# Kernel tuning notes

Hardware: AMD Instinct MI355X
Metric: run time of the kernel (lower is better)

## Reference

```python
import jax, jax.numpy as jnp
import numpy as np

ALPHA = 0.5      # GCN2Conv alpha
THETA = 1.0      # GCN2Conv theta (beta_l = log(theta/l + 1))
EPS = 1e-5       # pyg LayerNorm eps
N_LAYERS = 8
N, E, DIN, DHID, DOUT = 50000, 800000, 128, 256, 128


def setup_inputs() -> dict:
    key = jax.random.key(0)
    ks = jax.random.split(key, 10)
    x = jax.random.normal(ks[0], (N, DIN), jnp.float32)
    edge_index = jax.random.randint(ks[1], (2, E), 0, N, dtype=jnp.int32)
    lin1_w = jax.random.normal(ks[2], (DIN, DHID), jnp.float32) / np.sqrt(DIN)
    lin1_b = jnp.zeros((DHID,), jnp.float32)
    conv_w1 = jax.random.normal(ks[3], (N_LAYERS, DHID, DHID), jnp.float32) / np.sqrt(DHID)
    conv_w2 = jax.random.normal(ks[4], (N_LAYERS, DHID, DHID), jnp.float32) / np.sqrt(DHID)
    norm_gamma = jnp.ones((N_LAYERS, DHID), jnp.float32)
    norm_beta = jnp.zeros((N_LAYERS, DHID), jnp.float32)
    lin2_w = jax.random.normal(ks[5], (DHID, DOUT), jnp.float32) / np.sqrt(DHID)
    lin2_b = jnp.zeros((DOUT,), jnp.float32)
    return {"x": x, "edge_index": edge_index, "lin1_w": lin1_w, "lin1_b": lin1_b,
            "conv_w1": conv_w1, "conv_w2": conv_w2, "norm_gamma": norm_gamma,
            "norm_beta": norm_beta, "lin2_w": lin2_w, "lin2_b": lin2_b}


def _gcn_norm(edge_index, n_nodes, dtype):
    # add self loops, then symmetric deg^{-1/2} A_hat deg^{-1/2} normalization
    loop = jnp.arange(n_nodes, dtype=edge_index.dtype)
    row = jnp.concatenate([edge_index[0], loop])
    col = jnp.concatenate([edge_index[1], loop])
    deg = jax.ops.segment_sum(jnp.ones_like(row, dtype=dtype), col, num_segments=n_nodes)
    dis = jnp.where(deg > 0, jax.lax.rsqrt(jnp.maximum(deg, 1e-12)), 0.0)
    return row, col, dis[row] * dis[col]


def _graph_layernorm(h, gamma, beta):
    # pyg LayerNorm mode='graph', batch=None: normalize over all nodes+features
    z = h - jnp.mean(h)
    z = z / (jnp.sqrt(jnp.mean(z * z)) + EPS)
    return gamma * z + beta


def reference(x, edge_index, lin1_w, lin1_b, conv_w1, conv_w2, norm_gamma, norm_beta, lin2_w, lin2_b):
    n_nodes = x.shape[0]
    row, col, enorm = _gcn_norm(edge_index, n_nodes, x.dtype)
    # lin1 + relu (dropout p=0 -> identity); residual=None -> zeros
    x0 = jax.nn.relu(x @ lin1_w + lin1_b)
    h = x0
    for i in range(conv_w1.shape[0]):
        beta_l = float(np.log(THETA / (i + 1) + 1.0))
        # sparse neighborhood aggregation: out[c] += norm * h[r]
        agg = jax.ops.segment_sum(h[row] * enorm[:, None], col, num_segments=n_nodes)
        t = (1.0 - ALPHA) * agg          # propagated part
        r = ALPHA * x0                   # initial-residual part (res = x0 + zeros)
        # shared_weights=False: separate weights for propagated and residual parts
        h = (1.0 - beta_l) * (t + r) + beta_l * (t @ conv_w1[i] + r @ conv_w2[i])
        h = jax.nn.relu(_graph_layernorm(h, norm_gamma[i], norm_beta[i]))
    return jax.nn.relu(h @ lin2_w + lin2_b)
```

## Files before the change

kernel.cpp:

```cpp
#include <hip/hip_runtime.h>
#include <hip/hip_bf16.h>
#include <math.h>

#define DIN 128
#define DH 256
#define DOUT 128
#define NLAYERS 8
#define EPSLN 1e-5f

typedef __hip_bfloat16 bf16;
typedef __attribute__((ext_vector_type(8))) short short8;
typedef __attribute__((ext_vector_type(4))) short short4v;
typedef __attribute__((ext_vector_type(4))) float f32x4;

__device__ __forceinline__ float ldf(const void* p, size_t idx, int isbf) {
    if (isbf) return __bfloat162float(((const bf16*)p)[idx]);
    return ((const float*)p)[idx];
}
__device__ __forceinline__ short f2s(float v) {
    bf16 b = __float2bfloat16(v);
    return *reinterpret_cast<short*>(&b);
}
__device__ __forceinline__ float s2f(short s) {
    unsigned int u = ((unsigned int)(unsigned short)s) << 16;
    float f;
    __builtin_memcpy(&f, &u, 4);
    return f;
}
__device__ __forceinline__ void gl_lds16(const void* g, void* l) {
    __builtin_amdgcn_global_load_lds(
        (const __attribute__((address_space(1))) unsigned int*)g,
        (__attribute__((address_space(3))) unsigned int*)l,
        16, 0, 0);
}

__global__ void k_detect(const unsigned int* __restrict__ xw, int* __restrict__ flag) {
    __shared__ int cnt;
    if (threadIdx.x == 0) cnt = 0;
    __syncthreads();
    unsigned int w = xw[threadIdx.x];
    int e = (w >> 7) & 0xFF;
    if (e >= 112 && e <= 140) atomicAdd(&cnt, 1);
    __syncthreads();
    if (threadIdx.x == 0) *flag = (cnt >= 128) ? 1 : 0;
}

__global__ void k_init_cnt(int* __restrict__ cnt, int N) {
    int i = blockIdx.x * blockDim.x + threadIdx.x;
    if (i < N) cnt[i] = 0;
}
__global__ void k_count(const int* __restrict__ cols, int* __restrict__ cnt, int E) {
    int e = blockIdx.x * blockDim.x + threadIdx.x;
    if (e < E) atomicAdd(&cnt[cols[e]], 1);
}
__global__ void k_dis(const int* __restrict__ cnt, float* __restrict__ dis, int N) {
    int i = blockIdx.x * blockDim.x + threadIdx.x;
    if (i < N) dis[i] = rsqrtf(1.0f + (float)cnt[i]);
}
__global__ void k_scan1(const int* __restrict__ cnt, int* __restrict__ rowptr,
                        int* __restrict__ bsum, int N) {
    __shared__ int s[256];
    int t = threadIdx.x;
    int i = blockIdx.x * 256 + t;
    s[t] = (i < N) ? cnt[i] : 0;
    __syncthreads();
    for (int off = 1; off < 256; off <<= 1) {
        int x = (t >= off) ? s[t - off] : 0;
        __syncthreads();
        s[t] += x;
        __syncthreads();
    }
    if (i < N) rowptr[i + 1] = s[t];
    if (t == 255) bsum[blockIdx.x] = s[255];
}
__global__ void k_scan2(int* __restrict__ bsum, int nb) {
    __shared__ int s[256];
    int t = threadIdx.x;
    s[t] = (t < nb) ? bsum[t] : 0;
    __syncthreads();
    for (int off = 1; off < 256; off <<= 1) {
        int x = (t >= off) ? s[t - off] : 0;
        __syncthreads();
        s[t] += x;
        __syncthreads();
    }
    if (t < nb) bsum[t] = s[t];
}
__global__ void k_scan3(int* __restrict__ rowptr, const int* __restrict__ bsum, int N) {
    int i = blockIdx.x * 256 + threadIdx.x;
    if (i == 0) rowptr[0] = 0;
    if (i < N && blockIdx.x > 0) rowptr[i + 1] += bsum[blockIdx.x - 1];
}
__global__ void k_cursor(const int* __restrict__ rowptr, int* __restrict__ cursor, int N) {
    int i = blockIdx.x * 256 + threadIdx.x;
    if (i < N) cursor[i] = rowptr[i];
}
__global__ void k_fill(const int* __restrict__ rows, const int* __restrict__ cols,
                       int* __restrict__ cursor, int* __restrict__ csr, int E) {
    int e = blockIdx.x * blockDim.x + threadIdx.x;
    if (e < E) {
        int c = cols[e], r = rows[e];
        int pos = atomicAdd(&cursor[c], 1);
        csr[pos] = r;
    }
}

__global__ void k_zero_stats(float* __restrict__ stats) {
    int t = threadIdx.x;
    if (t < 16) stats[t] = 0.0f;
}

__global__ void k_transw2(const void* __restrict__ w1, const void* __restrict__ w2,
                          const int* __restrict__ flag, short* __restrict__ wt) {
    __shared__ float tile[32][33];
    int z = blockIdx.z;
    int lay = z >> 1, m = z & 1;
    const void* src = m ? w2 : w1;
    size_t sbase = (size_t)lay * 65536;
    short* dst = wt + (size_t)lay * 131072 + (size_t)m * 256;
    float bl = logf(1.0f / (float)(lay + 1) + 1.0f);
    float c0 = 0.5f * (1.0f - bl);
    float c1 = 0.5f * bl;
    int isbf = *flag;
    int tx = threadIdx.x, ty = threadIdx.y;
    int n0 = blockIdx.x * 32, k0 = blockIdx.y * 32;
    #pragma unroll
    for (int i = 0; i < 4; i++) {
        int k = k0 + ty + i * 8;
        tile[ty + i * 8][tx] = ldf(src, sbase + (size_t)k * 256 + n0 + tx, isbf);
    }
    __syncthreads();
    #pragma unroll
    for (int i = 0; i < 4; i++) {
        int n = n0 + ty + i * 8;
        int k = k0 + tx;
        float v = c1 * tile[tx][ty + i * 8];
        if (k == n) v += c0;
        dst[(size_t)n * 512 + k] = f2s(v);
    }
}

__global__ void k_transw_lin(const void* __restrict__ src, const int* __restrict__ flag,
                             short* __restrict__ dst, int K, int Nc) {
    __shared__ float tile[32][33];
    int isbf = *flag;
    int tx = threadIdx.x, ty = threadIdx.y;
    int n0 = blockIdx.x * 32, k0 = blockIdx.y * 32;
    #pragma unroll
    for (int i = 0; i < 4; i++) {
        int k = k0 + ty + i * 8;
        tile[ty + i * 8][tx] = ldf(src, (size_t)k * Nc + n0 + tx, isbf);
    }
    __syncthreads();
    #pragma unroll
    for (int i = 0; i < 4; i++) {
        int n = n0 + ty + i * 8;
        dst[(size_t)n * K + k0 + tx] = f2s(tile[tx][ty + i * 8]);
    }
}

__global__ void k_convx(const void* __restrict__ x, const int* __restrict__ flag,
                        short* __restrict__ xb, int total) {
    int i = blockIdx.x * 256 + threadIdx.x;
    if (i < total) xb[i] = f2s(ldf(x, i, *flag));
}

template<int BN, int KK, int FINAL>
__global__ __launch_bounds__(256) void gemm_mfma(
    const short* __restrict__ A, const short* __restrict__ wt,
    const void* __restrict__ bias, const int* __restrict__ flag,
    void* __restrict__ outp, int Nn)
{
    constexpr int NT = BN / 16;
    __shared__ __align__(16) short Atile[128 * 32];
    __shared__ __align__(16) short Btile[BN * 32];
    int t = threadIdx.x;
    int w = t >> 6, lane = t & 63;
    int lr = lane & 15, quad = lane >> 4;
    int row0 = blockIdx.x * 128;
    int sub = t & 3;
    int srow = t >> 2;
    f32x4 acc[2][NT];
    #pragma unroll
    for (int m = 0; m < 2; m++)
        #pragma unroll
        for (int nt = 0; nt < NT; nt++)
            #pragma unroll
            for (int j = 0; j < 4; j++) acc[m][nt][j] = 0.f;

    for (int kb = 0; kb < KK; kb += 32) {
        #pragma unroll
        for (int r = 0; r < 2; r++) {
            int gr = row0 + srow + r * 64;
            if (gr >= Nn) gr = Nn - 1;
            gl_lds16(A + (size_t)gr * KK + kb + sub * 8,
                     Atile + (size_t)(t + r * 256) * 8);
        }
        #pragma unroll
        for (int r = 0; r < BN / 64; r++) {
            int n = srow + r * 64;
            gl_lds16(wt + (size_t)n * KK + kb + sub * 8,
                     Btile + (size_t)(t + r * 256) * 8);
        }
        __syncthreads();
        short8 a0 = *(const short8*)(Atile + (w * 32 + lr) * 32 + quad * 8);
        short8 a1 = *(const short8*)(Atile + (w * 32 + 16 + lr) * 32 + quad * 8);
        #pragma unroll
        for (int nt = 0; nt < NT; nt++) {
            short8 bv = *(const short8*)(Btile + (nt * 16 + lr) * 32 + quad * 8);
            acc[0][nt] = __builtin_amdgcn_mfma_f32_16x16x32_bf16(a0, bv, acc[0][nt], 0, 0, 0);
            acc[1][nt] = __builtin_amdgcn_mfma_f32_16x16x32_bf16(a1, bv, acc[1][nt], 0, 0, 0);
        }
        __syncthreads();
    }
    const int isbf = *flag;
    #pragma unroll
    for (int m = 0; m < 2; m++) {
        #pragma unroll
        for (int nt = 0; nt < NT; nt++) {
            int gc = nt * 16 + lr;
            float bb = ldf(bias, gc, isbf);
            #pragma unroll
            for (int i = 0; i < 4; i++) {
                int gr = row0 + w * 32 + m * 16 + quad * 4 + i;
                if (gr < Nn) {
                    float v = acc[m][nt][i] + bb;
                    v = v > 0.f ? v : 0.f;
                    size_t off = (size_t)gr * BN + gc;
                    if (FINAL) {
                        if (isbf) ((bf16*)outp)[off] = __float2bfloat16(v);
                        else      ((float*)outp)[off] = v;
                    } else {
                        ((bf16*)outp)[off] = __float2bfloat16(v);
                    }
                }
            }
        }
    }
}

__global__ __launch_bounds__(256) void k_gather2(
    const int* __restrict__ rowptr, const int* __restrict__ csr,
    const float* __restrict__ dis, const bf16* __restrict__ hsrc,
    bf16* __restrict__ agg,
    const void* __restrict__ g, const void* __restrict__ b, size_t loff,
    const float* __restrict__ stats2, float invTotal, int useLN,
    const int* __restrict__ flag, int N)
{
    int gid = blockIdx.x * 256 + threadIdx.x;
    int node = gid >> 6;
    if (node >= N) return;
    int lane = gid & 63;
    int col = lane * 4;
    float cA[4], cB[4];
    if (useLN) {
        int isbf = *flag;
        float mu = stats2[0] * invTotal;
        float var = stats2[1] * invTotal - mu * mu;
        var = var > 0.f ? var : 0.f;
        float inv = 1.0f / (sqrtf(var) + EPSLN);
        #pragma unroll
        for (int j = 0; j < 4; j++) {
            float gg = ldf(g, loff + col + j, isbf);
            float bb = ldf(b, loff + col + j, isbf);
            cA[j] = gg * inv;
            cB[j] = fmaf(-gg * inv, mu, bb);
        }
    } else {
        #pragma unroll
        for (int j = 0; j < 4; j++) { cA[j] = 1.0f; cB[j] = 0.0f; }
    }
    const short* hs = (const short*)hsrc;
    float dc = dis[node];
    float acc[4], acc2[4];
    {
        short4v hv = *(const short4v*)(hs + (size_t)node * DH + col);
        #pragma unroll
        for (int j = 0; j < 4; j++) {
            float v = fmaf(cA[j], s2f(hv[j]), cB[j]);
            v = v > 0.f ? v : 0.f;
            acc[j] = dc * v;
            acc2[j] = 0.f;
        }
    }
    int i = rowptr[node], e1 = rowptr[node + 1];
    for (; i + 4 <= e1; i += 4) {
        int r0 = csr[i], r1 = csr[i + 1], r2 = csr[i + 2], r3 = csr[i + 3];
        float w0 = dis[r0], w1 = dis[r1], w2 = dis[r2], w3 = dis[r3];
        short4v v0 = *(const short4v*)(hs + (size_t)r0 * DH + col);
        short4v v1 = *(const short4v*)(hs + (size_t)r1 * DH + col);
        short4v v2 = *(const short4v*)(hs + (size_t)r2 * DH + col);
        short4v v3 = *(const short4v*)(hs + (size_t)r3 * DH + col);
        #pragma unroll
        for (int j = 0; j < 4; j++) {
            float a0 = fmaf(cA[j], s2f(v0[j]), cB[j]); a0 = a0 > 0.f ? a0 : 0.f;
            float a1 = fmaf(cA[j], s2f(v1[j]), cB[j]); a1 = a1 > 0.f ? a1 : 0.f;
            float a2 = fmaf(cA[j], s2f(v2[j]), cB[j]); a2 = a2 > 0.f ? a2 : 0.f;
            float a3 = fmaf(cA[j], s2f(v3[j]), cB[j]); a3 = a3 > 0.f ? a3 : 0.f;
            acc[j]  = fmaf(w0, a0, acc[j]);
            acc2[j] = fmaf(w1, a1, acc2[j]);
            acc[j]  = fmaf(w2, a2, acc[j]);
            acc2[j] = fmaf(w3, a3, acc2[j]);
        }
    }
    for (; i < e1; i++) {
        int r = csr[i];
        float wr = dis[r];
        short4v v0 = *(const short4v*)(hs + (size_t)r * DH + col);
        #pragma unroll
        for (int j = 0; j < 4; j++) {
            float a0 = fmaf(cA[j], s2f(v0[j]), cB[j]); a0 = a0 > 0.f ? a0 : 0.f;
            acc[j] = fmaf(wr, a0, acc[j]);
        }
    }
    short4v o;
    #pragma unroll
    for (int j = 0; j < 4; j++) o[j] = f2s(dc * (acc[j] + acc2[j]));
    *(short4v*)((short*)agg + (size_t)node * DH + col) = o;
}

__global__ __launch_bounds__(256) void gemm_layer3(
    const bf16* __restrict__ agg, const bf16* __restrict__ x0,
    const short* __restrict__ wt, bf16* __restrict__ h,
    float* __restrict__ stats2, int Nn)
{
    __shared__ __align__(16) short Atile[128 * 32];
    __shared__ __align__(16) short Btile[256 * 32];
    int t = threadIdx.x;
    int w = t >> 6, lane = t & 63;
    int lr = lane & 15, quad = lane >> 4;
    int row0 = blockIdx.x * 128;
    int sub = t & 3;
    int srow = t >> 2;
    f32x4 acc[2][16];
    #pragma unroll
    for (int m = 0; m < 2; m++)
        #pragma unroll
        for (int nt = 0; nt < 16; nt++)
            #pragma unroll
            for (int j = 0; j < 4; j++) acc[m][nt][j] = 0.f;

    for (int kb = 0; kb < 512; kb += 32) {
        const short* Asrc = (const short*)((kb < DH) ? agg : x0);
        int ka = kb & (DH - 1);
        #pragma unroll
        for (int r = 0; r < 2; r++) {
            int gr = row0 + srow + r * 64;
            if (gr >= Nn) gr = Nn - 1;
            gl_lds16(Asrc + (size_t)gr * DH + ka + sub * 8,
                     Atile + (size_t)(t + r * 256) * 8);
        }
        #pragma unroll
        for (int r = 0; r < 4; r++) {
            int n = srow + r * 64;
            gl_lds16(wt + (size_t)n * 512 + kb + sub * 8,
                     Btile + (size_t)(t + r * 256) * 8);
        }
        __syncthreads();
        short8 a0 = *(const short8*)(Atile + (w * 32 + lr) * 32 + quad * 8);
        short8 a1 = *(const short8*)(Atile + (w * 32 + 16 + lr) * 32 + quad * 8);
        #pragma unroll
        for (int nt = 0; nt < 16; nt++) {
            short8 bv = *(const short8*)(Btile + (nt * 16 + lr) * 32 + quad * 8);
            acc[0][nt] = __builtin_amdgcn_mfma_f32_16x16x32_bf16(a0, bv, acc[0][nt], 0, 0, 0);
            acc[1][nt] = __builtin_amdgcn_mfma_f32_16x16x32_bf16(a1, bv, acc[1][nt], 0, 0, 0);
        }
        __syncthreads();
    }
    float lsum = 0.f, lsq = 0.f;
    #pragma unroll
    for (int m = 0; m < 2; m++) {
        #pragma unroll
        for (int nt = 0; nt < 16; nt++) {
            int gc = nt * 16 + lr;
            #pragma unroll
            for (int i = 0; i < 4; i++) {
                int gr = row0 + w * 32 + m * 16 + quad * 4 + i;
                if (gr < Nn) {
                    float v = acc[m][nt][i];
                    h[(size_t)gr * DH + gc] = __float2bfloat16(v);
                    lsum += v;
                    lsq += v * v;
                }
            }
        }
    }
    float* red = (float*)Btile;
    red[t] = lsum;
    red[256 + t] = lsq;
    __syncthreads();
    for (int s = 128; s > 0; s >>= 1) {
        if (t < s) { red[t] += red[t + s]; red[256 + t] += red[256 + t + s]; }
        __syncthreads();
    }
    if (t == 0) {
        atomicAdd(&stats2[0], red[0]);
        atomicAdd(&stats2[1], red[256]);
    }
}

__global__ __launch_bounds__(256) void k_applyT(
    bf16* __restrict__ h, const float* __restrict__ stats2, float invTotal,
    const void* __restrict__ g, const void* __restrict__ b, size_t loff,
    const int* __restrict__ flag, int total)
{
    int idx = blockIdx.x * 256 + threadIdx.x;
    if (idx >= total) return;
    const int isbf = *flag;
    float mu = stats2[0] * invTotal;
    float var = stats2[1] * invTotal - mu * mu;
    var = var > 0.f ? var : 0.f;
    float inv = 1.0f / (sqrtf(var) + EPSLN);
    int j = idx & (DH - 1);
    float gg = ldf(g, loff + j, isbf);
    float bb = ldf(b, loff + j, isbf);
    float v = fmaf(gg * inv, __bfloat162float(h[idx]), fmaf(-gg * inv, mu, bb));
    v = v > 0.f ? v : 0.f;
    h[idx] = __float2bfloat16(v);
}

extern "C" void kernel_launch(void* const* d_in, const int* in_sizes, int n_in,
                              void* d_out, int out_size, void* d_ws, size_t ws_size,
                              hipStream_t stream) {
    const void* x      = d_in[0];
    const int*  ei     = (const int*)d_in[1];
    const void* lin1_w = d_in[2];
    const void* lin1_b = d_in[3];
    const void* conv_w1= d_in[4];
    const void* conv_w2= d_in[5];
    const void* gam    = d_in[6];
    const void* bet    = d_in[7];
    const void* lin2_w = d_in[8];
    const void* lin2_b = d_in[9];

    const int N = in_sizes[0] / DIN;
    const int E = in_sizes[1] / 2;
    const int* rows = ei;
    const int* cols = ei + E;
    const size_t NDH = (size_t)N * DH;
    const size_t Nr = ((size_t)N + 255) / 256 * 256;

    char* p = (char*)d_ws;
    auto alloc = [&](size_t bytes) { char* q = p; p += (bytes + 255) & ~(size_t)255; return q; };
    float* dis    = (float*)alloc(Nr * 4);
    float* stats  = (float*)alloc(1024);
    int*   flag   = (int*)(stats + 16);
    int*   cnt    = (int*)alloc(Nr * 4);
    int*   rowptr = (int*)alloc((Nr + 256) * 4);
    int*   cursor = (int*)alloc(Nr * 4);
    int*   bsum   = (int*)alloc(1024);
    int*   csr    = (int*)alloc((size_t)E * 4);
    short* wt     = (short*)alloc((size_t)NLAYERS * 131072 * 2);
    short* w1t    = (short*)alloc((size_t)DH * DIN * 2);
    short* w2t    = (short*)alloc((size_t)DOUT * DH * 2);
    short* xb     = (short*)alloc((size_t)N * DIN * 2);
    bf16*  agg    = (bf16*)alloc(NDH * 2);
    bf16*  x0     = (bf16*)alloc(NDH * 2);
    bf16*  h      = (bf16*)alloc(NDH * 2);

    dim3 blk(256);
    int nbN = (N + 255) / 256;
    dim3 gN(nbN);
    dim3 gE((E + 255) / 256);
    dim3 gB((N + 127) / 128);
    dim3 gG((N + 3) / 4);
    dim3 gElem((unsigned)((NDH + 255) / 256));
    dim3 gTW(8, 8, 16);
    dim3 bTW(32, 8);

    k_detect<<<1, 256, 0, stream>>>((const unsigned int*)x, flag);
    k_init_cnt<<<gN, blk, 0, stream>>>(cnt, N);
    k_count<<<gE, blk, 0, stream>>>(cols, cnt, E);
    k_dis<<<gN, blk, 0, stream>>>(cnt, dis, N);
    k_scan1<<<gN, blk, 0, stream>>>(cnt, rowptr, bsum, N);
    k_scan2<<<1, 256, 0, stream>>>(bsum, nbN);
    k_scan3<<<gN, blk, 0, stream>>>(rowptr, bsum, N);
    k_cursor<<<gN, blk, 0, stream>>>(rowptr, cursor, N);
    k_fill<<<gE, blk, 0, stream>>>(rows, cols, cursor, csr, E);
    k_zero_stats<<<1, 64, 0, stream>>>(stats);
    k_transw2<<<gTW, bTW, 0, stream>>>(conv_w1, conv_w2, flag, wt);
    k_transw_lin<<<dim3(DH / 32, DIN / 32), bTW, 0, stream>>>(lin1_w, flag, w1t, DIN, DH);
    k_transw_lin<<<dim3(DOUT / 32, DH / 32), bTW, 0, stream>>>(lin2_w, flag, w2t, DH, DOUT);
    k_convx<<<dim3((unsigned)(((size_t)N * DIN + 255) / 256)), blk, 0, stream>>>(x, flag, xb, N * DIN);

    gemm_mfma<DH, DIN, 0><<<gB, blk, 0, stream>>>(xb, w1t, lin1_b, flag, x0, N);

    const float invTotal = 1.0f / ((float)N * (float)DH);
    for (int l = 0; l < NLAYERS; l++) {
        const bf16* hsrc = (l == 0) ? x0 : h;
        size_t loff = (l == 0) ? 0 : (size_t)(l - 1) * DH;
        const float* st = (l == 0) ? stats : stats + 2 * (l - 1);
        k_gather2<<<gG, blk, 0, stream>>>(rowptr, csr, dis, hsrc, agg,
                                          gam, bet, loff, st, invTotal,
                                          l > 0 ? 1 : 0, flag, N);
        gemm_layer3<<<gB, blk, 0, stream>>>(agg, x0, wt + (size_t)l * 131072,
                                            h, stats + 2 * l, N);
    }
    k_applyT<<<gElem, blk, 0, stream>>>(h, stats + 2 * (NLAYERS - 1), invTotal,
                                        gam, bet, (size_t)(NLAYERS - 1) * DH,
                                        flag, (int)NDH);
    gemm_mfma<DOUT, DH, 1><<<gB, blk, 0, stream>>>((const short*)h, w2t, lin2_b,
                                                   flag, d_out, N);
}
```

Before: 1.276 ms.

## Use 512-thread GEMM blocks with fragment-ordered LDS tiles and shuffle reduction

```diff
diff --git a/kernel.cpp b/kernel.cpp
--- a/kernel.cpp
+++ b/kernel.cpp
@@ -166,73 +166,64 @@
 }
 
 template<int BN, int KK, int FINAL>
-__global__ __launch_bounds__(256) void gemm_mfma(
+__global__ __launch_bounds__(512, 4) void gemm_mfma(
     const short* __restrict__ A, const short* __restrict__ wt,
     const void* __restrict__ bias, const int* __restrict__ flag,
     void* __restrict__ outp, int Nn)
 {
     constexpr int NT = BN / 16;
+    constexpr int BROUNDS = BN / 128;
     __shared__ __align__(16) short Atile[128 * 32];
     __shared__ __align__(16) short Btile[BN * 32];
     int t = threadIdx.x;
     int w = t >> 6, lane = t & 63;
     int lr = lane & 15, quad = lane >> 4;
     int row0 = blockIdx.x * 128;
-    int sub = t & 3;
-    int srow = t >> 2;
-    f32x4 acc[2][NT];
-    #pragma unroll
-    for (int m = 0; m < 2; m++)
-        #pragma unroll
-        for (int nt = 0; nt < NT; nt++)
-            #pragma unroll
-            for (int j = 0; j < 4; j++) acc[m][nt][j] = 0.f;
+    int sf = t >> 6;
+    int srow = lane & 15;
+    int skq = lane >> 4;
+    f32x4 acc[NT];
+    #pragma unroll
+    for (int nt = 0; nt < NT; nt++)
+        #pragma unroll
+        for (int j = 0; j < 4; j++) acc[nt][j] = 0.f;
 
     for (int kb = 0; kb < KK; kb += 32) {
-        #pragma unroll
-        for (int r = 0; r < 2; r++) {
-            int gr = row0 + srow + r * 64;
-            if (gr >= Nn) gr = Nn - 1;
-            gl_lds16(A + (size_t)gr * KK + kb + sub * 8,
-                     Atile + (size_t)(t + r * 256) * 8);
-        }
-        #pragma unroll
-        for (int r = 0; r < BN / 64; r++) {
-            int n = srow + r * 64;
-            gl_lds16(wt + (size_t)n * KK + kb + sub * 8,
-                     Btile + (size_t)(t + r * 256) * 8);
-        }
-        __syncthreads();
-        short8 a0 = *(const short8*)(Atile + (w * 32 + lr) * 32 + quad * 8);
-        short8 a1 = *(const short8*)(Atile + (w * 32 + 16 + lr) * 32 + quad * 8);
+        int gr = row0 + sf * 16 + srow;
+        if (gr >= Nn) gr = Nn - 1;
+        gl_lds16(A + (size_t)gr * KK + kb + skq * 8, Atile + (size_t)t * 8);
+        #pragma unroll
+        for (int r = 0; r < BROUNDS; r++) {
+            int n = (sf + r * 8) * 16 + srow;
+            gl_lds16(wt + (size_t)n * KK + kb + skq * 8,
+                     Btile + (size_t)(t + r * 512) * 8);
+        }
+        __syncthreads();
+        short8 a = *(const short8*)(Atile + w * 512 + lane * 8);
         #pragma unroll
         for (int nt = 0; nt < NT; nt++) {
-            short8 bv = *(const short8*)(Btile + (nt * 16 + lr) * 32 + quad * 8);
-            acc[0][nt] = __builtin_amdgcn_mfma_f32_16x16x32_bf16(a0, bv, acc[0][nt], 0, 0, 0);
-            acc[1][nt] = __builtin_amdgcn_mfma_f32_16x16x32_bf16(a1, bv, acc[1][nt], 0, 0, 0);
+            short8 bv = *(const short8*)(Btile + nt * 512 + lane * 8);
+            acc[nt] = __builtin_amdgcn_mfma_f32_16x16x32_bf16(a, bv, acc[nt], 0, 0, 0);
         }
         __syncthreads();
     }
     const int isbf = *flag;
     #pragma unroll
-    for (int m = 0; m < 2; m++) {
-        #pragma unroll
-        for (int nt = 0; nt < NT; nt++) {
-            int gc = nt * 16 + lr;
-            float bb = ldf(bias, gc, isbf);
-            #pragma unroll
-            for (int i = 0; i < 4; i++) {
-                int gr = row0 + w * 32 + m * 16 + quad * 4 + i;
-                if (gr < Nn) {
-                    float v = acc[m][nt][i] + bb;
-                    v = v > 0.f ? v : 0.f;
-                    size_t off = (size_t)gr * BN + gc;
-                    if (FINAL) {
-                        if (isbf) ((bf16*)outp)[off] = __float2bfloat16(v);
-                        else      ((float*)outp)[off] = v;
-                    } else {
-                        ((bf16*)outp)[off] = __float2bfloat16(v);
-                    }
+    for (int nt = 0; nt < NT; nt++) {
+        int gc = nt * 16 + lr;
+        float bb = ldf(bias, gc, isbf);
+        #pragma unroll
+        for (int i = 0; i < 4; i++) {
+            int gr = row0 + w * 16 + quad * 4 + i;
+            if (gr < Nn) {
+                float v = acc[nt][i] + bb;
+                v = v > 0.f ? v : 0.f;
+                size_t off = (size_t)gr * BN + gc;
+                if (FINAL) {
+                    if (isbf) ((bf16*)outp)[off] = __float2bfloat16(v);
+                    else      ((float*)outp)[off] = v;
+                } else {
+                    ((bf16*)outp)[off] = __float2bfloat16(v);
                 }
             }
         }
@@ -319,87 +310,80 @@
     *(short4v*)((short*)agg + (size_t)node * DH + col) = o;
 }
 
-__global__ __launch_bounds__(256) void gemm_layer3(
+__global__ __launch_bounds__(512, 4) void gemm_layer3(
     const bf16* __restrict__ agg, const bf16* __restrict__ x0,
     const short* __restrict__ wt, bf16* __restrict__ h,
     float* __restrict__ stats2, int Nn)
 {
     __shared__ __align__(16) short Atile[128 * 32];
     __shared__ __align__(16) short Btile[256 * 32];
+    __shared__ float sred[16];
     int t = threadIdx.x;
     int w = t >> 6, lane = t & 63;
     int lr = lane & 15, quad = lane >> 4;
     int row0 = blockIdx.x * 128;
-    int sub = t & 3;
-    int srow = t >> 2;
-    f32x4 acc[2][16];
-    #pragma unroll
-    for (int m = 0; m < 2; m++)
-        #pragma unroll
-        for (int nt = 0; nt < 16; nt++)
-            #pragma unroll
-            for (int j = 0; j < 4; j++) acc[m][nt][j] = 0.f;
+    int sf = t >> 6;
+    int srow = lane & 15;
+    int skq = lane >> 4;
+    f32x4 acc[16];
+    #pragma unroll
+    for (int nt = 0; nt < 16; nt++)
+        #pragma unroll
+        for (int j = 0; j < 4; j++) acc[nt][j] = 0.f;
 
     for (int kb = 0; kb < 512; kb += 32) {
         const short* Asrc = (const short*)((kb < DH) ? agg : x0);
-        int ka = kb & (DH - 1);
+        int ka = (kb & (DH - 1)) + skq * 8;
+        int gr = row0 + sf * 16 + srow;
+        if (gr >= Nn) gr = Nn - 1;
+        gl_lds16(Asrc + (size_t)gr * DH + ka, Atile + (size_t)t * 8);
         #pragma unroll
         for (int r = 0; r < 2; r++) {
-            int gr = row0 + srow + r * 64;
-            if (gr >= Nn) gr = Nn - 1;
-            gl_lds16(Asrc + (size_t)gr * DH + ka + sub * 8,
-                     Atile + (size_t)(t + r * 256) * 8);
-        }
-        #pragma unroll
-        for (int r = 0; r < 4; r++) {
-            int n = srow + r * 64;
-            gl_lds16(wt + (size_t)n * 512 + kb + sub * 8,
-                     Btile + (size_t)(t + r * 256) * 8);
-        }
-        __syncthreads();
-        short8 a0 = *(const short8*)(Atile + (w * 32 + lr) * 32 + quad * 8);
-        short8 a1 = *(const short8*)(Atile + (w * 32 + 16 + lr) * 32 + quad * 8);
+            int n = (sf + r * 8) * 16 + srow;
+            gl_lds16(wt + (size_t)n * 512 + kb + skq * 8,
+                     Btile + (size_t)(t + r * 512) * 8);
+        }
+        __syncthreads();
+        short8 a = *(const short8*)(Atile + w * 512 + lane * 8);
         #pragma unroll
         for (int nt = 0; nt < 16; nt++) {
-            short8 bv = *(const short8*)(Btile + (nt * 16 + lr) * 32 + quad * 8);
-            acc[0][nt] = __builtin_amdgcn_mfma_f32_16x16x32_bf16(a0, bv, acc[0][nt], 0, 0, 0);
-            acc[1][nt] = __builtin_amdgcn_mfma_f32_16x16x32_bf16(a1, bv, acc[1][nt], 0, 0, 0);
+            short8 bv = *(const short8*)(Btile + nt * 512 + lane * 8);
+            acc[nt] = __builtin_amdgcn_mfma_f32_16x16x32_bf16(a, bv, acc[nt], 0, 0, 0);
         }
         __syncthreads();
     }
     float lsum = 0.f, lsq = 0.f;
     #pragma unroll
-    for (int m = 0; m < 2; m++) {
-        #pragma unroll
-        for (int nt = 0; nt < 16; nt++) {
-            int gc = nt * 16 + lr;
-            #pragma unroll
-            for (int i = 0; i < 4; i++) {
-                int gr = row0 + w * 32 + m * 16 + quad * 4 + i;
-                if (gr < Nn) {
-                    float v = acc[m][nt][i];
-                    h[(size_t)gr * DH + gc] = __float2bfloat16(v);
-                    lsum += v;
-                    lsq += v * v;
-                }
+    for (int nt = 0; nt < 16; nt++) {
+        int gc = nt * 16 + lr;
+        #pragma unroll
+        for (int i = 0; i < 4; i++) {
+            int gr = row0 + w * 16 + quad * 4 + i;
+            if (gr < Nn) {
+                float v = acc[nt][i];
+                h[(size_t)gr * DH + gc] = __float2bfloat16(v);
+                lsum += v;
+                lsq += v * v;
             }
         }
     }
-    float* red = (float*)Btile;
-    red[t] = lsum;
-    red[256 + t] = lsq;
-    __syncthreads();
-    for (int s = 128; s > 0; s >>= 1) {
-        if (t < s) { red[t] += red[t + s]; red[256 + t] += red[256 + t + s]; }
-        __syncthreads();
-    }
+    #pragma unroll
+    for (int off = 32; off > 0; off >>= 1) {
+        lsum += __shfl_down(lsum, off);
+        lsq  += __shfl_down(lsq, off);
+    }
+    if (lane == 0) { sred[w] = lsum; sred[8 + w] = lsq; }
+    __syncthreads();
     if (t == 0) {
-        atomicAdd(&stats2[0], red[0]);
-        atomicAdd(&stats2[1], red[256]);
-    }
-}
-
-__global__ __launch_bounds__(256) void k_applyT(
+        float s0 = 0.f, s1 = 0.f;
+        #pragma unroll
+        for (int i = 0; i < 8; i++) { s0 += sred[i]; s1 += sred[8 + i]; }
+        atomicAdd(&stats2[0], s0);
+        atomicAdd(&stats2[1], s1);
+    }
+}
+
+__global__ void k_applyT(
     bf16* __restrict__ h, const float* __restrict__ stats2, float invTotal,
     const void* __restrict__ g, const void* __restrict__ b, size_t loff,
     const int* __restrict__ flag, int total)
@@ -467,6 +451,7 @@
     dim3 gElem((unsigned)((NDH + 255) / 256));
     dim3 gTW(8, 8, 16);
     dim3 bTW(32, 8);
+    dim3 blk512(512);
 
     k_detect<<<1, 256, 0, stream>>>((const unsigned int*)x, flag);
     k_init_cnt<<<gN, blk, 0, stream>>>(cnt, N);
@@ -483,7 +468,7 @@
     k_transw_lin<<<dim3(DOUT / 32, DH / 32), bTW, 0, stream>>>(lin2_w, flag, w2t, DH, DOUT);
     k_convx<<<dim3((unsigned)(((size_t)N * DIN + 255) / 256)), blk, 0, stream>>>(x, flag, xb, N * DIN);
 
-    gemm_mfma<DH, DIN, 0><<<gB, blk, 0, stream>>>(xb, w1t, lin1_b, flag, x0, N);
+    gemm_mfma<DH, DIN, 0><<<gB, blk512, 0, stream>>>(xb, w1t, lin1_b, flag, x0, N);
 
     const float invTotal = 1.0f / ((float)N * (float)DH);
     for (int l = 0; l < NLAYERS; l++) {
@@ -493,12 +478,12 @@
         k_gather2<<<gG, blk, 0, stream>>>(rowptr, csr, dis, hsrc, agg,
                                           gam, bet, loff, st, invTotal,
                                           l > 0 ? 1 : 0, flag, N);
-        gemm_layer3<<<gB, blk, 0, stream>>>(agg, x0, wt + (size_t)l * 131072,
-                                            h, stats + 2 * l, N);
+        gemm_layer3<<<gB, blk512, 0, stream>>>(agg, x0, wt + (size_t)l * 131072,
+                                               h, stats + 2 * l, N);
     }
     k_applyT<<<gElem, blk, 0, stream>>>(h, stats + 2 * (NLAYERS - 1), invTotal,
                                         gam, bet, (size_t)(NLAYERS - 1) * DH,
                                         flag, (int)NDH);
-    gemm_mfma<DOUT, DH, 1><<<gB, blk, 0, stream>>>((const short*)h, w2t, lin2_b,
-                                                   flag, d_out, N);
-}
+    gemm_mfma<DOUT, DH, 1><<<gB, blk512, 0, stream>>>((const short*)h, w2t, lin2_b,
+                                                      flag, d_out, N);
+}
```

Measured after the change: 1.112 ms. 1.15x faster.
